# Kernel tuning notes

Hardware: AMD Instinct MI355X
Metric: run time of the kernel (lower is better)

## Reference

```python
import jax, jax.numpy as jnp
import numpy as np

PRIOR = 0.1      # prior_prob
P_NOISE = 0.05   # p
DAMPING = 0.5
BETA = 0.3
EPS = 1e-10


def compute_likelihood(Y_edges, prod_fail_others, beta_edges, p):
    p_sick_if_healthy = 1.0 - prod_fail_others
    p_sick_if_infected = 1.0 - prod_fail_others * (1.0 - beta_edges)
    normal_if_sick = (1.0 - p) * p_sick_if_healthy
    sick_if_sick = (1.0 - p) * p_sick_if_infected
    normal_if_normal = p * p_sick_if_healthy + (1.0 - p_sick_if_healthy)
    sick_if_normal = p * p_sick_if_infected + (1.0 - p_sick_if_infected)
    is_pos = Y_edges == 1
    L0 = jnp.where(is_pos, normal_if_sick, normal_if_normal)
    L1 = jnp.where(is_pos, sick_if_sick, sick_if_normal)
    return L0, L1


def setup_inputs() -> dict:
    key = jax.random.key(0)
    k1, k2, k3 = jax.random.split(key, 3)
    num_tests = 100000
    num_patients = 200000
    num_edges = 12800000
    Y_obs = jax.random.randint(k1, (num_tests,), 0, 2, dtype=jnp.int32)
    idx_i = jax.random.randint(k2, (num_edges,), 0, num_tests, dtype=jnp.int32)
    idx_j = jax.random.randint(k3, (num_edges,), 0, num_patients, dtype=jnp.int32)
    # beta_edges = 1.0 on diagonal entries, beta elsewhere (as in __init__)
    beta_edges = jnp.where(idx_i == idx_j, 1.0, BETA).astype(jnp.float32)
    return {"Y_obs": Y_obs, "idx_i": idx_i, "idx_j": idx_j,
            "beta_edges": beta_edges, "max_iters": 50,
            "num_patients": num_patients}


def reference(Y_obs, idx_i, idx_j, beta_edges, max_iters, num_patients):
    num_tests = Y_obs.shape[0]
    num_edges = idx_i.shape[0]
    Y_edges = Y_obs[idx_i]  # [E]

    def step(carry, it):
        msg_j_to_i, old0, old1, _ = carry
        # test-side aggregation: prob all other patients failed to infect test i
        fail = 1.0 - beta_edges * msg_j_to_i
        log_fail = jnp.log(fail + EPS)
        tot_log_fail = jax.ops.segment_sum(log_fail, idx_i, num_segments=num_tests)
        prod_fail_others = jnp.exp(tot_log_fail[idx_i]) / (fail + EPS)
        new0, new1 = compute_likelihood(Y_edges, prod_fail_others, beta_edges, P_NOISE)
        first = it == 0
        m0 = jnp.where(first, new0, DAMPING * new0 + (1.0 - DAMPING) * old0)
        m1 = jnp.where(first, new1, DAMPING * new1 + (1.0 - DAMPING) * old1)
        old0_n, old1_n = m0, m1  # stored BEFORE normalization, as in torch code
        norm = m0 + m1 + EPS
        log_m0 = jnp.log(m0 / norm + EPS)
        log_m1 = jnp.log(m1 / norm + EPS)
        # patient-side aggregation
        t0 = jax.ops.segment_sum(log_m0, idx_j, num_segments=num_patients)
        t1 = jax.ops.segment_sum(log_m1, idx_j, num_segments=num_patients)
        log_b0 = jnp.log(1.0 - PRIOR) + t0
        log_b1 = jnp.log(PRIOR) + t1
        beliefs = jax.nn.sigmoid(log_b1 - log_b0)  # = 1/(1+exp(lb0-lb1))
        msg_next = jax.nn.sigmoid((log_b1[idx_j] - log_m1) - (log_b0[idx_j] - log_m0))
        return (msg_next, old0_n, old1_n, beliefs), None

    init = (jnp.full((num_edges,), PRIOR, dtype=jnp.float32),
            jnp.zeros((num_edges,), jnp.float32),
            jnp.zeros((num_edges,), jnp.float32),
            jnp.full((num_patients,), PRIOR, dtype=jnp.float32))
    (_, _, _, node_beliefs), _ = jax.lax.scan(step, init, jnp.arange(max_iters))
    return node_beliefs
```

## Files before the change

### kernel.cpp

```cpp
#include <hip/hip_runtime.h>
#include <hip/hip_fp16.h>

#define EPSF   1e-10f
#define PRIORF 0.1f
#define QF     0.95f
#define BETAF  0.3f
#define BS     256
#define WPB    4
#define CAPT   4
#define LOGIT_PRIOR (-2.1972245773362196f)
#define GSH    13
#define NG_MAX 32
#define SPAN_I 256
#define NB2_MAX 1024
#define SPAN_J 128
#define NBJ_MAX 2048
#define CHA    8192
#define CHB    8192
#define CHJ    8192
#define D16    0x2000u
#define JL16   0x1FFFu
#define NXCD   8
#define BSP    1024
#define WPBP   32
#define BLK_SLP 256

__device__ __forceinline__ float wave_sum(float v) {
    #pragma unroll
    for (int m = 32; m >= 1; m >>= 1) v += __shfl_xor(v, m, 64);
    return v;
}
__device__ __forceinline__ float frcp(float x) {
    return __builtin_amdgcn_rcpf(x);
}
__device__ __forceinline__ float2 unpack(__half2 h) {
    return make_float2(__low2float(h), __high2float(h));
}
__device__ __forceinline__ float calcD(float2 o) {
    float inv = frcp(o.x + o.y + EPSF);
    return __logf(o.y * inv + EPSF) - __logf(o.x * inv + EPSF);
}
__device__ __forceinline__ float sigmoidf(float x) {
    return frcp(1.0f + __expf(-x));
}

__device__ __forceinline__ int run_search(int cum, int len, int v0,
                                          int cidx, int NG, int* gout) {
    int lo = 0, hi = NG - 1;
    #pragma unroll
    for (int st = 0; st < 5; ++st) {
        int mid = (lo + hi) >> 1;
        int cmid = __shfl(cum, mid);
        int open = (lo < hi);
        int p = (cmid > cidx);
        int nhi = p ? mid : hi;
        int nlo = p ? lo : (mid + 1);
        hi = open ? nhi : hi;
        lo = open ? nlo : lo;
    }
    int cl = __shfl(cum, lo);
    int ll = __shfl(len, lo);
    int vv = __shfl(v0, lo);
    *gout = lo;
    return vv + cidx - (cl - ll);
}

__global__ __launch_bounds__(BS) void k_test(
    const int*            __restrict__ rowptrG,
    const unsigned short* __restrict__ jidx16,
    const int*            __restrict__ Y,
    const float*          __restrict__ delta,
    __half2*              __restrict__ oldm,
    int T, int NG, int first, int BPC)
{
    int lane = threadIdx.x & 63;
    int x  = blockIdx.x & (NXCD - 1);
    int mm = blockIdx.x >> 3;
    int i = (x * BPC + mm) * WPB + (threadIdx.x >> 6);
    if (i >= T) return;
    int v0 = 0, v1 = 0;
    if (lane < NG) v0 = rowptrG[(size_t)i * NG + lane];
    int l2 = lane - 32;
    if (l2 >= 0 && l2 < NG) v1 = rowptrG[(size_t)(i + 1) * NG + l2];
    int endv = __shfl(v1, 32 + lane);
    int len = (lane < NG) ? (endv - v0) : 0;
    int cum = len;
    #pragma unroll
    for (int off = 1; off < 64; off <<= 1) {
        int t = __shfl_up(cum, off);
        if (lane >= off) cum += t;
    }
    int deg = __shfl(cum, 63);
    int nch = (deg + 63) >> 6;
    int ypos = (Y[i] == 1);
    float lsum = 0.0f;

    if (deg <= 64 * CAPT) {
        int ssv[CAPT]; int ksv[CAPT]; float2 osv[CAPT]; float fsv[CAPT];
        #pragma unroll
        for (int c = 0; c < CAPT; ++c) {
            if (c >= nch) break;
            int idx = c * 64 + lane;
            int cidx = min(idx, deg - 1);
            int g;
            int s = run_search(cum, len, v0, cidx, NG, &g);
            bool act = (idx < deg);
            int k = 0; float2 o = make_float2(0.f, 0.f); float f = 1.0f;
            if (act) {
                k = jidx16[s];
                float b = (k & D16) ? 1.0f : BETAF;
                float msg;
                if (first) msg = PRIORF;
                else {
                    o = unpack(oldm[s]);
                    int j = (g << GSH) | (k & JL16);
                    msg = sigmoidf(delta[j] - calcD(o));
                }
                f = 1.0f - b * msg;
                lsum += __logf(f + EPSF);
            }
            ssv[c] = act ? s : -1; ksv[c] = k; osv[c] = o; fsv[c] = f;
        }
        float Etot = __expf(wave_sum(lsum));
        #pragma unroll
        for (int c = 0; c < CAPT; ++c) {
            if (c >= nch) break;
            int s = ssv[c];
            if (s < 0) continue;
            int k = ksv[c]; float f = fsv[c];
            float b = (k & D16) ? 1.0f : BETAF;
            float prod = Etot * frcp(f + EPSF);
            float psh = 1.0f - prod;
            float psi = 1.0f - prod * (1.0f - b);
            float L0 = ypos ? QF * psh : 1.0f - QF * psh;
            float L1 = ypos ? QF * psi : 1.0f - QF * psi;
            float m0, m1;
            if (first) { m0 = L0; m1 = L1; }
            else { float2 o = osv[c]; m0 = 0.5f * L0 + 0.5f * o.x;
                                      m1 = 0.5f * L1 + 0.5f * o.y; }
            oldm[s] = __floats2half2_rn(m0, m1);
        }
    } else {
        for (int base = 0; base < deg; base += 64) {
            int idx = base + lane;
            int cidx = min(idx, deg - 1);
            int g;
            int s = run_search(cum, len, v0, cidx, NG, &g);
            if (idx < deg) {
                int k = jidx16[s];
                float b = (k & D16) ? 1.0f : BETAF;
                float msg;
                if (first) msg = PRIORF;
                else {
                    int j = (g << GSH) | (k & JL16);
                    msg = sigmoidf(delta[j] - calcD(unpack(oldm[s])));
                }
                lsum += __logf(1.0f - b * msg + EPSF);
            }
        }
        float Etot = __expf(wave_sum(lsum));
        for (int base = 0; base < deg; base += 64) {
            int idx = base + lane;
            int cidx = min(idx, deg - 1);
            int g;
            int s = run_search(cum, len, v0, cidx, NG, &g);
            if (idx < deg) {
                int k = jidx16[s];
                float b = (k & D16) ? 1.0f : BETAF;
                float2 o = make_float2(0.f, 0.f);
                float msg;
                if (first) msg = PRIORF;
                else { o = unpack(oldm[s]);
                       int j = (g << GSH) | (k & JL16);
                       msg = sigmoidf(delta[j] - calcD(o)); }
                float f = 1.0f - b * msg;
                float prod = Etot * frcp(f + EPSF);
                float psh = 1.0f - prod;
                float psi = 1.0f - prod * (1.0f - b);
                float L0 = ypos ? QF * psh : 1.0f - QF * psh;
                float L1 = ypos ? QF * psi : 1.0f - QF * psi;
                float m0, m1;
                if (first) { m0 = L0; m1 = L1; }
                else { m0 = 0.5f * L0 + 0.5f * o.x; m1 = 0.5f * L1 + 0.5f * o.y; }
                oldm[s] = __floats2half2_rn(m0, m1);
            }
        }
    }
}

__global__ __launch_bounds__(BSP) void k_patient(
    const int*     __restrict__ colptr,
    const int*     __restrict__ eposJ,
    const __half2* __restrict__ oldm,
    float*         __restrict__ delta,
    float*         __restrict__ out, int P, int NG)
{
    int b = blockIdx.x;
    int x = b & (NXCD - 1);
    int r = b >> 3;
    int m = r >> 8;
    int w = r & (BLK_SLP - 1);
    int g = x + NXCD * m;
    if (g >= NG) return;
    int lane = threadIdx.x & 63;
    int hl = lane & 31;
    int p = (g << GSH) + w * WPBP + ((threadIdx.x >> 6) << 1) + (lane >> 5);
    if (p >= P) return;
    int u0 = colptr[p], u1 = colptr[p + 1];
    float S = 0.0f;
    for (int u = u0 + hl; u < u1; u += 32)
        S += calcD(unpack(oldm[eposJ[u]]));
    #pragma unroll
    for (int mm = 16; mm >= 1; mm >>= 1) S += __shfl_xor(S, mm, 64);
    if (hl == 0) {
        float d = LOGIT_PRIOR + S;
        delta[p] = d;
        out[p] = sigmoidf(d);
    }
}

__global__ void k_zf2(int* frontG, int* front2, int* frontJ,
                      int NG, int nb2tot, int nbj) {
    int t = blockIdx.x * blockDim.x + threadIdx.x;
    if (t <= NG) frontG[t] = 0;
    if (t <= nb2tot) front2[t] = 0;
    if (t <= nbj) frontJ[t] = 0;
}

__global__ __launch_bounds__(BS) void k_binG(
    const int* __restrict__ idx_i, const int* __restrict__ idx_j,
    int* __restrict__ frontG, unsigned* __restrict__ stageA,
    int E, int NG, int capA)
{
    __shared__ int h[NG_MAX], rsv[NG_MAX], cu[NG_MAX];
    int tid = threadIdx.x;
    if (tid < NG) h[tid] = 0;
    __syncthreads();
    int start = blockIdx.x * CHA, end = min(start + CHA, E);
    for (int e = start + tid; e < end; e += BS)
        atomicAdd(&h[idx_j[e] >> GSH], 1);
    __syncthreads();
    if (tid < NG) { int c = h[tid];
        rsv[tid] = c ? atomicAdd(&frontG[tid], c) : 0; cu[tid] = 0; }
    __syncthreads();
    for (int e = start + tid; e < end; e += BS) {
        int i = idx_i[e], j = idx_j[e];
        int g = j >> GSH;
        int pos = rsv[g] + atomicAdd(&cu[g], 1);
        if (pos < capA)
            stageA[(size_t)g * capA + pos] =
                ((unsigned)i << 14) | ((unsigned)(i == j) << 13)
                | (unsigned)(j & ((1 << GSH) - 1));
    }
}

__global__ __launch_bounds__(BS) void k_binI2(
    const unsigned* __restrict__ stageA, const int* __restrict__ frontG,
    int* __restrict__ front2, unsigned* __restrict__ stage2,
    int NG, int NB2, int capA, int cap2, int chunks)
{
    int g = blockIdx.x / chunks, c = blockIdx.x % chunks;
    int n = min(frontG[g], capA);
    int start = c * 2 * CHB, end = min(start + 2 * CHB, n);
    if (start >= end) return;
    __shared__ int h[NB2_MAX], rsv[NB2_MAX], cu[NB2_MAX];
    int tid = threadIdx.x;
    for (int b = tid; b < NB2; b += BS) h[b] = 0;
    __syncthreads();
    const unsigned* rb = stageA + (size_t)g * capA;
    for (int r = start + tid; r < end; r += BS)
        atomicAdd(&h[(rb[r] >> 14) >> 8], 1);
    __syncthreads();
    for (int b = tid; b < NB2; b += BS) {
        int cc = h[b];
        rsv[b] = cc ? atomicAdd(&front2[g * NB2 + b], cc) : 0;
        cu[b] = 0;
    }
    __syncthreads();
    for (int r = start + tid; r < end; r += BS) {
        unsigned v = rb[r];
        int i = (int)(v >> 14);
        int ib = i >> 8;
        int pos = rsv[ib] + atomicAdd(&cu[ib], 1);
        if (pos < cap2)
            stage2[(size_t)(g * NB2 + ib) * cap2 + pos] =
                ((unsigned)(i & 255) << 14) | (v & 0x3FFFu);
    }
}

__global__ void k_scan_front(int* a, int n, int cap) {
    __shared__ int tmp[BS];
    __shared__ int carry;
    int tid = threadIdx.x;
    if (tid == 0) carry = 0;
    __syncthreads();
    for (int base = 0; base < n; base += BS) {
        int i = base + tid;
        int v = (i < n) ? min(a[i], cap) : 0;
        tmp[tid] = v; __syncthreads();
        for (int off = 1; off < BS; off <<= 1) {
            int x = (tid >= off) ? tmp[tid - off] : 0;
            __syncthreads();
            tmp[tid] += x;
            __syncthreads();
        }
        int c = carry;
        if (i < n) a[i] = c + tmp[tid] - v;
        __syncthreads();
        if (tid == BS - 1) carry = c + tmp[tid];
        __syncthreads();
    }
    if (tid == 0) a[n] = carry;
}

__global__ __launch_bounds__(BS) void k_csr2(
    const unsigned* __restrict__ stage2, const int* __restrict__ front2s,
    int* __restrict__ rowptrG, unsigned short* __restrict__ jidx16,
    int T, int NG, int NB2, int cap2)
{
    __shared__ int deg[SPAN_I], loff[SPAN_I], cu[SPAN_I];
    int b = blockIdx.x, tid = threadIdx.x;
    int g = b / NB2, ib = b % NB2;
    int base = front2s[b];
    int n = min(front2s[b + 1] - base, cap2);
    deg[tid] = 0;
    __syncthreads();
    const unsigned* rb = stage2 + (size_t)b * cap2;
    for (int r = tid; r < n; r += BS)
        atomicAdd(&deg[rb[r] >> 14], 1);
    __syncthreads();
    loff[tid] = deg[tid];
    __syncthreads();
    for (int off = 1; off < SPAN_I; off <<= 1) {
        int v = (tid >= off) ? loff[tid - off] : 0;
        __syncthreads();
        loff[tid] += v;
        __syncthreads();
    }
    {
        int excl = loff[tid] - deg[tid];
        int i = ib * SPAN_I + tid;
        if (i < T) rowptrG[(size_t)i * NG + g] = base + excl;
        cu[tid] = base + excl;
    }
    __syncthreads();
    for (int r = tid; r < n; r += BS) {
        unsigned v = rb[r];
        int pos = atomicAdd(&cu[v >> 14], 1);
        jidx16[pos] = (unsigned short)(v & 0x3FFFu);
    }
}

__global__ void k_fin(const int* front2s, int* rowptrG, int T, int NG, int NB2) {
    int g = threadIdx.x;
    if (g < NG) rowptrG[(size_t)T * NG + g] = front2s[(g + 1) * NB2];
}

__global__ __launch_bounds__(BS) void k_binJ(
    const unsigned short* __restrict__ jidx16,
    const int* __restrict__ front2s,
    int* __restrict__ front, unsigned int* __restrict__ stage,
    int E, int nbj, int cap, int NG, int NB2)
{
    __shared__ int h[NBJ_MAX], rsv[NBJ_MAX], cu[NBJ_MAX];
    __shared__ int ends[NG_MAX];
    int tid = threadIdx.x;
    if (tid < NG) ends[tid] = front2s[(tid + 1) * NB2];
    for (int b = tid; b < nbj; b += BS) h[b] = 0;
    __syncthreads();
    int start = blockIdx.x * CHJ, end = min(start + CHJ, E);
    for (int e = start + tid; e < end; e += BS) {
        int lo = 0, hi = NG - 1;
        while (lo < hi) { int mid = (lo + hi) >> 1;
                          if (e < ends[mid]) hi = mid; else lo = mid + 1; }
        int j = (lo << GSH) | (jidx16[e] & JL16);
        atomicAdd(&h[j >> 7], 1);
    }
    __syncthreads();
    for (int b = tid; b < nbj; b += BS) {
        int c = h[b];
        rsv[b] = c ? atomicAdd(&front[b], c) : 0;
        cu[b] = 0;
    }
    __syncthreads();
    for (int e = start + tid; e < end; e += BS) {
        int lo = 0, hi = NG - 1;
        while (lo < hi) { int mid = (lo + hi) >> 1;
                          if (e < ends[mid]) hi = mid; else lo = mid + 1; }
        int j = (lo << GSH) | (jidx16[e] & JL16);
        int bb = j >> 7;
        int pos = rsv[bb] + atomicAdd(&cu[bb], 1);
        if (pos < cap)
            stage[(size_t)bb * cap + pos] = ((unsigned)(j & 127) << 24) | (unsigned)e;
    }
}

__global__ __launch_bounds__(BS) void k_csrJ(
    const unsigned int* __restrict__ stage, const int* __restrict__ fbase,
    int* __restrict__ colptr, int* __restrict__ eposJ, int P, int E, int cap)
{
    __shared__ int deg[SPAN_J], loff[SPAN_J], cu[SPAN_J];
    int b = blockIdx.x, tid = threadIdx.x;
    int gbase = fbase[b];
    int n = min(fbase[b + 1] - gbase, cap);
    if (tid < SPAN_J) deg[tid] = 0;
    __syncthreads();
    const unsigned int* rb = stage + (size_t)b * cap;
    for (int r = tid; r < n; r += BS)
        atomicAdd(&deg[rb[r] >> 24], 1);
    __syncthreads();
    if (tid < SPAN_J) loff[tid] = deg[tid];
    __syncthreads();
    for (int off = 1; off < SPAN_J; off <<= 1) {
        int v = 0;
        if (tid < SPAN_J && tid >= off) v = loff[tid - off];
        __syncthreads();
        if (tid < SPAN_J) loff[tid] += v;
        __syncthreads();
    }
    if (tid < SPAN_J) {
        int excl = loff[tid] - deg[tid];
        int p = b * SPAN_J + tid;
        if (p < P) colptr[p] = gbase + excl;
        cu[tid] = gbase + excl;
    }
    __syncthreads();
    for (int r = tid; r < n; r += BS) {
        unsigned int v = rb[r];
        int pos = atomicAdd(&cu[v >> 24], 1);
        eposJ[pos] = (int)(v & 0xFFFFFFu);
    }
    if (b == 0 && tid == 0) colptr[P] = E;
}

extern "C" void kernel_launch(void* const* d_in, const int* in_sizes, int n_in,
                              void* d_out, int out_size, void* d_ws, size_t ws_size,
                              hipStream_t stream) {
    const int* Y     = (const int*)d_in[0];
    const int* idx_i = (const int*)d_in[1];
    const int* idx_j = (const int*)d_in[2];
    const int T = in_sizes[0];
    const int E = in_sizes[1];
    const int P = out_size;
    const int ITERS = 50;

    int* eposJ = (int*)d_in[3];

    const int NG     = (P + (1 << GSH) - 1) >> GSH;
    const int NB2    = (T + SPAN_I - 1) / SPAN_I;
    const int nb2tot = NG * NB2;
    const int nbj    = (P + SPAN_J - 1) / SPAN_J;
    long long meanA = (long long)E * (1 << GSH) / P;
    const int capA  = (int)(meanA + (meanA >> 6) + 4096);
    long long mean2 = meanA * SPAN_I / T;
    const int cap2  = (int)(mean2 + (mean2 >> 4) + 256);
    const int capJ  = E / nbj + E / (nbj * 8) + 1024;

    char* ws = (char*)d_ws;
    auto alloc = [&](size_t bytes) -> char* {
        char* p = ws; ws += (bytes + 255) & ~(size_t)255; return p;
    };
    int* rowptrG = (int*)alloc((size_t)(T + 1) * NG * 4);
    int* colptr  = (int*)alloc((size_t)(P + 1) * 4);
    int* frontG  = (int*)alloc((size_t)(NG + 1) * 4);
    int* front2  = (int*)alloc((size_t)(nb2tot + 1) * 4);
    int* frontJ  = (int*)alloc((size_t)(nbj + 1) * 4);
    size_t szA = (size_t)capA * NG * 4, szjx = (size_t)E * 2;
    char* regionA = alloc(szA > szjx ? szA : szjx);
    unsigned*       stageA = (unsigned*)regionA;
    unsigned short* jidx16 = (unsigned short*)regionA;
    size_t oldm_b = ((size_t)E * 4 + 255) & ~(size_t)255;
    size_t sz2 = (size_t)cap2 * nb2tot * 4;
    size_t szJ = (size_t)capJ * nbj * 4;
    size_t szO = oldm_b + (size_t)P * 4;
    size_t szB = sz2 > szJ ? sz2 : szJ; if (szO > szB) szB = szO;
    char* regionB = alloc(szB);
    unsigned* stage2 = (unsigned*)regionB;
    unsigned* stageJ = (unsigned*)regionB;
    __half2*  oldm   = (__half2*)regionB;
    float*    delta  = (float*)(regionB + oldm_b);
    float*    out    = (float*)d_out;

    const int zb = (nb2tot + BS) / BS + 1;
    const int chunks = (capA + 2 * CHB - 1) / (2 * CHB);
    k_zf2<<<zb, BS, 0, stream>>>(frontG, front2, frontJ, NG, nb2tot, nbj);
    k_binG<<<(E + CHA - 1) / CHA, BS, 0, stream>>>(idx_i, idx_j, frontG, stageA,
                                                   E, NG, capA);
    k_binI2<<<NG * chunks, BS, 0, stream>>>(stageA, frontG, front2, stage2,
                                            NG, NB2, capA, cap2, chunks);
    k_scan_front<<<1, BS, 0, stream>>>(front2, nb2tot, cap2);
    k_csr2<<<nb2tot, BS, 0, stream>>>(stage2, front2, rowptrG, jidx16,
                                      T, NG, NB2, cap2);
    k_fin<<<1, 64, 0, stream>>>(front2, rowptrG, T, NG, NB2);
    k_binJ<<<(E + CHJ - 1) / CHJ, BS, 0, stream>>>(jidx16, front2, frontJ, stageJ,
                                                   E, nbj, capJ, NG, NB2);
    k_scan_front<<<1, BS, 0, stream>>>(frontJ, nbj, capJ);
    k_csrJ<<<nbj, BS, 0, stream>>>(stageJ, frontJ, colptr, eposJ, P, E, capJ);

    const int BPC   = (T + WPB * NXCD - 1) / (WPB * NXCD);
    const int tgrid = NXCD * BPC;
    const int maxm  = (NG + NXCD - 1) / NXCD;
    const int pgrid = NXCD * maxm * BLK_SLP;
    for (int it = 0; it < ITERS; ++it) {
        k_test<<<tgrid, BS, 0, stream>>>(rowptrG, jidx16, Y, delta, oldm,
                                         T, NG, it == 0, BPC);
        k_patient<<<pgrid, BSP, 0, stream>>>(colptr, eposJ, oldm, delta, out,
                                             P, NG);
    }
}
```

Before: 8.482 ms.

## Precompute per-edge patient messages in patient kernel and pack diagonal flags into bits

The patient kernel now makes a second pass over each patient's edges and writes a per-edge float prem = belief logit minus own message. The test kernel then reads that value directly instead of gathering delta[j] at random and decoding jidx16. Diagonal flags are compacted into a bitmask so jidx16 no longer has to be read each iteration, and its buffer is reused to hold prem. The cost is an extra scattered write of E floats plus a re-read of oldm in the patient kernel, in exchange for removing the random delta gather. CHB is also doubled.

```diff
diff --git a/kernel.cpp b/kernel.cpp
--- a/kernel.cpp
+++ b/kernel.cpp
@@ -16,7 +16,7 @@
 #define SPAN_J 128
 #define NBJ_MAX 2048
 #define CHA    8192
-#define CHB    8192
+#define CHB    16384
 #define CHJ    8192
 #define D16    0x2000u
 #define JL16   0x1FFFu
@@ -66,11 +66,11 @@
 }
 
 __global__ __launch_bounds__(BS) void k_test(
-    const int*            __restrict__ rowptrG,
-    const unsigned short* __restrict__ jidx16,
-    const int*            __restrict__ Y,
-    const float*          __restrict__ delta,
-    __half2*              __restrict__ oldm,
+    const int*      __restrict__ rowptrG,
+    const unsigned* __restrict__ diagbits,
+    const float*    __restrict__ prem,
+    const int*      __restrict__ Y,
+    __half2*        __restrict__ oldm,
     int T, int NG, int first, int BPC)
 {
     int lane = threadIdx.x & 63;
@@ -96,7 +96,7 @@
     float lsum = 0.0f;
 
     if (deg <= 64 * CAPT) {
-        int ssv[CAPT]; int ksv[CAPT]; float2 osv[CAPT]; float fsv[CAPT];
+        int ssv[CAPT]; unsigned kv[CAPT]; float fsv[CAPT];
         #pragma unroll
         for (int c = 0; c < CAPT; ++c) {
             if (c >= nch) break;
@@ -105,21 +105,17 @@
             int g;
             int s = run_search(cum, len, v0, cidx, NG, &g);
             bool act = (idx < deg);
-            int k = 0; float2 o = make_float2(0.f, 0.f); float f = 1.0f;
+            unsigned diag = 0; float f = 1.0f;
             if (act) {
-                k = jidx16[s];
-                float b = (k & D16) ? 1.0f : BETAF;
+                diag = (diagbits[s >> 5] >> (s & 31)) & 1u;
+                float b = diag ? 1.0f : BETAF;
                 float msg;
                 if (first) msg = PRIORF;
-                else {
-                    o = unpack(oldm[s]);
-                    int j = (g << GSH) | (k & JL16);
-                    msg = sigmoidf(delta[j] - calcD(o));
-                }
+                else       msg = sigmoidf(prem[s]);
                 f = 1.0f - b * msg;
                 lsum += __logf(f + EPSF);
             }
-            ssv[c] = act ? s : -1; ksv[c] = k; osv[c] = o; fsv[c] = f;
+            ssv[c] = act ? s : -1; kv[c] = diag; fsv[c] = f;
         }
         float Etot = __expf(wave_sum(lsum));
         #pragma unroll
@@ -127,8 +123,8 @@
             if (c >= nch) break;
             int s = ssv[c];
             if (s < 0) continue;
-            int k = ksv[c]; float f = fsv[c];
-            float b = (k & D16) ? 1.0f : BETAF;
+            float f = fsv[c];
+            float b = kv[c] ? 1.0f : BETAF;
             float prod = Etot * frcp(f + EPSF);
             float psh = 1.0f - prod;
             float psi = 1.0f - prod * (1.0f - b);
@@ -136,8 +132,9 @@
             float L1 = ypos ? QF * psi : 1.0f - QF * psi;
             float m0, m1;
             if (first) { m0 = L0; m1 = L1; }
-            else { float2 o = osv[c]; m0 = 0.5f * L0 + 0.5f * o.x;
-                                      m1 = 0.5f * L1 + 0.5f * o.y; }
+            else { float2 o = unpack(oldm[s]);
+                   m0 = 0.5f * L0 + 0.5f * o.x;
+                   m1 = 0.5f * L1 + 0.5f * o.y; }
             oldm[s] = __floats2half2_rn(m0, m1);
         }
     } else {
@@ -147,14 +144,11 @@
             int g;
             int s = run_search(cum, len, v0, cidx, NG, &g);
             if (idx < deg) {
-                int k = jidx16[s];
-                float b = (k & D16) ? 1.0f : BETAF;
+                unsigned diag = (diagbits[s >> 5] >> (s & 31)) & 1u;
+                float b = diag ? 1.0f : BETAF;
                 float msg;
                 if (first) msg = PRIORF;
-                else {
-                    int j = (g << GSH) | (k & JL16);
-                    msg = sigmoidf(delta[j] - calcD(unpack(oldm[s])));
-                }
+                else       msg = sigmoidf(prem[s]);
                 lsum += __logf(1.0f - b * msg + EPSF);
             }
         }
@@ -165,14 +159,11 @@
             int g;
             int s = run_search(cum, len, v0, cidx, NG, &g);
             if (idx < deg) {
-                int k = jidx16[s];
-                float b = (k & D16) ? 1.0f : BETAF;
-                float2 o = make_float2(0.f, 0.f);
+                unsigned diag = (diagbits[s >> 5] >> (s & 31)) & 1u;
+                float b = diag ? 1.0f : BETAF;
                 float msg;
                 if (first) msg = PRIORF;
-                else { o = unpack(oldm[s]);
-                       int j = (g << GSH) | (k & JL16);
-                       msg = sigmoidf(delta[j] - calcD(o)); }
+                else       msg = sigmoidf(prem[s]);
                 float f = 1.0f - b * msg;
                 float prod = Etot * frcp(f + EPSF);
                 float psh = 1.0f - prod;
@@ -181,7 +172,8 @@
                 float L1 = ypos ? QF * psi : 1.0f - QF * psi;
                 float m0, m1;
                 if (first) { m0 = L0; m1 = L1; }
-                else { m0 = 0.5f * L0 + 0.5f * o.x; m1 = 0.5f * L1 + 0.5f * o.y; }
+                else { float2 o = unpack(oldm[s]);
+                       m0 = 0.5f * L0 + 0.5f * o.x; m1 = 0.5f * L1 + 0.5f * o.y; }
                 oldm[s] = __floats2half2_rn(m0, m1);
             }
         }
@@ -192,7 +184,7 @@
     const int*     __restrict__ colptr,
     const int*     __restrict__ eposJ,
     const __half2* __restrict__ oldm,
-    float*         __restrict__ delta,
+    float*         __restrict__ prem,
     float*         __restrict__ out, int P, int NG)
 {
     int b = blockIdx.x;
@@ -212,10 +204,11 @@
         S += calcD(unpack(oldm[eposJ[u]]));
     #pragma unroll
     for (int mm = 16; mm >= 1; mm >>= 1) S += __shfl_xor(S, mm, 64);
-    if (hl == 0) {
-        float d = LOGIT_PRIOR + S;
-        delta[p] = d;
-        out[p] = sigmoidf(d);
+    float d = LOGIT_PRIOR + S;
+    if (hl == 0) out[p] = sigmoidf(d);
+    for (int u = u0 + hl; u < u1; u += 32) {
+        int s = eposJ[u];
+        prem[s] = d - calcD(unpack(oldm[s]));
     }
 }
 
@@ -356,6 +349,16 @@
     if (g < NG) rowptrG[(size_t)T * NG + g] = front2s[(g + 1) * NB2];
 }
 
+__global__ __launch_bounds__(BS) void k_bits(
+    const unsigned short* __restrict__ jidx16,
+    unsigned long long*   __restrict__ diagbits64, int E)
+{
+    int e = blockIdx.x * BS + threadIdx.x;
+    unsigned short v = (e < E) ? jidx16[e] : (unsigned short)0;
+    unsigned long long m = __ballot((v >> 13) & 1);
+    if ((threadIdx.x & 63) == 0 && e < E) diagbits64[e >> 6] = m;
+}
+
 __global__ __launch_bounds__(BS) void k_binJ(
     const unsigned short* __restrict__ jidx16,
     const int* __restrict__ front2s,
@@ -465,20 +468,23 @@
     int* frontG  = (int*)alloc((size_t)(NG + 1) * 4);
     int* front2  = (int*)alloc((size_t)(nb2tot + 1) * 4);
     int* frontJ  = (int*)alloc((size_t)(nbj + 1) * 4);
-    size_t szA = (size_t)capA * NG * 4, szjx = (size_t)E * 2;
-    char* regionA = alloc(szA > szjx ? szA : szjx);
+    char* dbp = alloc((((size_t)E + 63) / 64) * 8);
+    unsigned long long* diagbits64 = (unsigned long long*)dbp;
+    unsigned*           diagbits32 = (unsigned*)dbp;
+    size_t szA = (size_t)capA * NG * 4, szjx = (size_t)E * 2, szpr = (size_t)E * 4;
+    size_t szRA = szA > szjx ? szA : szjx; if (szpr > szRA) szRA = szpr;
+    char* regionA = alloc(szRA);
     unsigned*       stageA = (unsigned*)regionA;
     unsigned short* jidx16 = (unsigned short*)regionA;
-    size_t oldm_b = ((size_t)E * 4 + 255) & ~(size_t)255;
+    float*          prem   = (float*)regionA;
+    size_t oldm_b = (size_t)E * 4;
     size_t sz2 = (size_t)cap2 * nb2tot * 4;
     size_t szJ = (size_t)capJ * nbj * 4;
-    size_t szO = oldm_b + (size_t)P * 4;
-    size_t szB = sz2 > szJ ? sz2 : szJ; if (szO > szB) szB = szO;
+    size_t szB = sz2 > szJ ? sz2 : szJ; if (oldm_b > szB) szB = oldm_b;
     char* regionB = alloc(szB);
     unsigned* stage2 = (unsigned*)regionB;
     unsigned* stageJ = (unsigned*)regionB;
     __half2*  oldm   = (__half2*)regionB;
-    float*    delta  = (float*)(regionB + oldm_b);
     float*    out    = (float*)d_out;
 
     const int zb = (nb2tot + BS) / BS + 1;
@@ -496,15 +502,16 @@
                                                    E, nbj, capJ, NG, NB2);
     k_scan_front<<<1, BS, 0, stream>>>(frontJ, nbj, capJ);
     k_csrJ<<<nbj, BS, 0, stream>>>(stageJ, frontJ, colptr, eposJ, P, E, capJ);
+    k_bits<<<(E + BS - 1) / BS, BS, 0, stream>>>(jidx16, diagbits64, E);
 
     const int BPC   = (T + WPB * NXCD - 1) / (WPB * NXCD);
     const int tgrid = NXCD * BPC;
     const int maxm  = (NG + NXCD - 1) / NXCD;
     const int pgrid = NXCD * maxm * BLK_SLP;
     for (int it = 0; it < ITERS; ++it) {
-        k_test<<<tgrid, BS, 0, stream>>>(rowptrG, jidx16, Y, delta, oldm,
+        k_test<<<tgrid, BS, 0, stream>>>(rowptrG, diagbits32, prem, Y, oldm,
                                          T, NG, it == 0, BPC);
-        k_patient<<<pgrid, BSP, 0, stream>>>(colptr, eposJ, oldm, delta, out,
+        k_patient<<<pgrid, BSP, 0, stream>>>(colptr, eposJ, oldm, prem, out,
                                              P, NG);
     }
 }
```

Result: slower. 15.14 ms (+78.5%).

## Process tests in 256-row blocks with shared-memory delta tiles and LDS atomics

Applied to the files above, without the earlier changes.

Replaces the wave-per-test kernel with a block that handles 256 tests at once. For each patient group it stages the delta slice (8192 floats) into shared memory and walks that group's edges in order, accumulating per-test log sums with shared-memory atomics through a new per-edge 8-bit local test index. The goal is to drop the per-edge binary search and turn random global delta gathers into LDS reads. In exchange it adds an extra byte array written during CSR build, repeated delta tile loads per block and group (done twice), LDS atomic contention, and many block-wide syncs. CHB is also doubled.

```diff
diff --git a/kernel.cpp b/kernel.cpp
--- a/kernel.cpp
+++ b/kernel.cpp
@@ -6,8 +6,8 @@
 #define QF     0.95f
 #define BETAF  0.3f
 #define BS     256
-#define WPB    4
-#define CAPT   4
+#define BST    1024
+#define TPB2   256
 #define LOGIT_PRIOR (-2.1972245773362196f)
 #define GSH    13
 #define NG_MAX 32
@@ -16,7 +16,7 @@
 #define SPAN_J 128
 #define NBJ_MAX 2048
 #define CHA    8192
-#define CHB    8192
+#define CHB    16384
 #define CHJ    8192
 #define D16    0x2000u
 #define JL16   0x1FFFu
@@ -25,11 +25,6 @@
 #define WPBP   32
 #define BLK_SLP 256
 
-__device__ __forceinline__ float wave_sum(float v) {
-    #pragma unroll
-    for (int m = 32; m >= 1; m >>= 1) v += __shfl_xor(v, m, 64);
-    return v;
-}
 __device__ __forceinline__ float frcp(float x) {
     return __builtin_amdgcn_rcpf(x);
 }
@@ -44,147 +39,87 @@
     return frcp(1.0f + __expf(-x));
 }
 
-__device__ __forceinline__ int run_search(int cum, int len, int v0,
-                                          int cidx, int NG, int* gout) {
-    int lo = 0, hi = NG - 1;
-    #pragma unroll
-    for (int st = 0; st < 5; ++st) {
-        int mid = (lo + hi) >> 1;
-        int cmid = __shfl(cum, mid);
-        int open = (lo < hi);
-        int p = (cmid > cidx);
-        int nhi = p ? mid : hi;
-        int nlo = p ? lo : (mid + 1);
-        hi = open ? nhi : hi;
-        lo = open ? nlo : lo;
-    }
-    int cl = __shfl(cum, lo);
-    int ll = __shfl(len, lo);
-    int vv = __shfl(v0, lo);
-    *gout = lo;
-    return vv + cidx - (cl - ll);
-}
-
-__global__ __launch_bounds__(BS) void k_test(
+__global__ __launch_bounds__(BST) void k_test2(
     const int*            __restrict__ rowptrG,
     const unsigned short* __restrict__ jidx16,
+    const unsigned char*  __restrict__ ilocal8,
     const int*            __restrict__ Y,
     const float*          __restrict__ delta,
     __half2*              __restrict__ oldm,
-    int T, int NG, int first, int BPC)
-{
-    int lane = threadIdx.x & 63;
-    int x  = blockIdx.x & (NXCD - 1);
-    int mm = blockIdx.x >> 3;
-    int i = (x * BPC + mm) * WPB + (threadIdx.x >> 6);
-    if (i >= T) return;
-    int v0 = 0, v1 = 0;
-    if (lane < NG) v0 = rowptrG[(size_t)i * NG + lane];
-    int l2 = lane - 32;
-    if (l2 >= 0 && l2 < NG) v1 = rowptrG[(size_t)(i + 1) * NG + l2];
-    int endv = __shfl(v1, 32 + lane);
-    int len = (lane < NG) ? (endv - v0) : 0;
-    int cum = len;
-    #pragma unroll
-    for (int off = 1; off < 64; off <<= 1) {
-        int t = __shfl_up(cum, off);
-        if (lane >= off) cum += t;
-    }
-    int deg = __shfl(cum, 63);
-    int nch = (deg + 63) >> 6;
-    int ypos = (Y[i] == 1);
-    float lsum = 0.0f;
-
-    if (deg <= 64 * CAPT) {
-        int ssv[CAPT]; int ksv[CAPT]; float2 osv[CAPT]; float fsv[CAPT];
-        #pragma unroll
-        for (int c = 0; c < CAPT; ++c) {
-            if (c >= nch) break;
-            int idx = c * 64 + lane;
-            int cidx = min(idx, deg - 1);
-            int g;
-            int s = run_search(cum, len, v0, cidx, NG, &g);
-            bool act = (idx < deg);
-            int k = 0; float2 o = make_float2(0.f, 0.f); float f = 1.0f;
-            if (act) {
-                k = jidx16[s];
-                float b = (k & D16) ? 1.0f : BETAF;
-                float msg;
-                if (first) msg = PRIORF;
-                else {
-                    o = unpack(oldm[s]);
-                    int j = (g << GSH) | (k & JL16);
-                    msg = sigmoidf(delta[j] - calcD(o));
-                }
-                f = 1.0f - b * msg;
-                lsum += __logf(f + EPSF);
-            }
-            ssv[c] = act ? s : -1; ksv[c] = k; osv[c] = o; fsv[c] = f;
+    int T, int NG, int P, int first, int BPB)
+{
+    __shared__ float dl[1 << GSH];
+    __shared__ float ls[TPB2];
+    __shared__ float et[TPB2];
+    __shared__ int   yb[TPB2];
+    __shared__ int   sgs[NG_MAX], sge[NG_MAX];
+    int tid = threadIdx.x;
+    int x = blockIdx.x & (NXCD - 1), mm = blockIdx.x >> 3;
+    int ib = x * BPB + mm;
+    int i0 = ib * TPB2;
+    if (i0 >= T) return;
+    int i1 = min(i0 + TPB2, T);
+    if (tid < NG) {
+        sgs[tid] = rowptrG[(size_t)i0 * NG + tid];
+        sge[tid] = rowptrG[(size_t)i1 * NG + tid];
+    }
+    if (tid < TPB2) {
+        ls[tid] = 0.0f;
+        yb[tid] = (i0 + tid < T) ? (Y[i0 + tid] == 1) : 0;
+    }
+    __syncthreads();
+
+    for (int g = 0; g < NG; ++g) {
+        if (!first) {
+            int jb = g << GSH;
+            for (int t = tid; t < (1 << GSH); t += BST)
+                dl[t] = (jb + t < P) ? delta[jb + t] : 0.0f;
+            __syncthreads();
         }
-        float Etot = __expf(wave_sum(lsum));
-        #pragma unroll
-        for (int c = 0; c < CAPT; ++c) {
-            if (c >= nch) break;
-            int s = ssv[c];
-            if (s < 0) continue;
-            int k = ksv[c]; float f = fsv[c];
+        int s0 = sgs[g], s1 = sge[g];
+        for (int s = s0 + tid; s < s1; s += BST) {
+            int k  = jidx16[s];
+            int il = ilocal8[s];
             float b = (k & D16) ? 1.0f : BETAF;
-            float prod = Etot * frcp(f + EPSF);
+            float msg = first ? PRIORF
+                : sigmoidf(dl[k & JL16] - calcD(unpack(oldm[s])));
+            atomicAdd(&ls[il], __logf(1.0f - b * msg + EPSF));
+        }
+        __syncthreads();
+    }
+    if (tid < TPB2) et[tid] = __expf(ls[tid]);
+    __syncthreads();
+
+    for (int g = 0; g < NG; ++g) {
+        if (!first) {
+            int jb = g << GSH;
+            for (int t = tid; t < (1 << GSH); t += BST)
+                dl[t] = (jb + t < P) ? delta[jb + t] : 0.0f;
+            __syncthreads();
+        }
+        int s0 = sgs[g], s1 = sge[g];
+        for (int s = s0 + tid; s < s1; s += BST) {
+            int k  = jidx16[s];
+            int il = ilocal8[s];
+            float b = (k & D16) ? 1.0f : BETAF;
+            float2 o = make_float2(0.f, 0.f);
+            float msg;
+            if (first) msg = PRIORF;
+            else { o = unpack(oldm[s]);
+                   msg = sigmoidf(dl[k & JL16] - calcD(o)); }
+            float f = 1.0f - b * msg;
+            float prod = et[il] * frcp(f + EPSF);
             float psh = 1.0f - prod;
             float psi = 1.0f - prod * (1.0f - b);
-            float L0 = ypos ? QF * psh : 1.0f - QF * psh;
-            float L1 = ypos ? QF * psi : 1.0f - QF * psi;
+            int yp = yb[il];
+            float L0 = yp ? QF * psh : 1.0f - QF * psh;
+            float L1 = yp ? QF * psi : 1.0f - QF * psi;
             float m0, m1;
             if (first) { m0 = L0; m1 = L1; }
-            else { float2 o = osv[c]; m0 = 0.5f * L0 + 0.5f * o.x;
-                                      m1 = 0.5f * L1 + 0.5f * o.y; }
+            else { m0 = 0.5f * L0 + 0.5f * o.x; m1 = 0.5f * L1 + 0.5f * o.y; }
             oldm[s] = __floats2half2_rn(m0, m1);
         }
-    } else {
-        for (int base = 0; base < deg; base += 64) {
-            int idx = base + lane;
-            int cidx = min(idx, deg - 1);
-            int g;
-            int s = run_search(cum, len, v0, cidx, NG, &g);
-            if (idx < deg) {
-                int k = jidx16[s];
-                float b = (k & D16) ? 1.0f : BETAF;
-                float msg;
-                if (first) msg = PRIORF;
-                else {
-                    int j = (g << GSH) | (k & JL16);
-                    msg = sigmoidf(delta[j] - calcD(unpack(oldm[s])));
-                }
-                lsum += __logf(1.0f - b * msg + EPSF);
-            }
-        }
-        float Etot = __expf(wave_sum(lsum));
-        for (int base = 0; base < deg; base += 64) {
-            int idx = base + lane;
-            int cidx = min(idx, deg - 1);
-            int g;
-            int s = run_search(cum, len, v0, cidx, NG, &g);
-            if (idx < deg) {
-                int k = jidx16[s];
-                float b = (k & D16) ? 1.0f : BETAF;
-                float2 o = make_float2(0.f, 0.f);
-                float msg;
-                if (first) msg = PRIORF;
-                else { o = unpack(oldm[s]);
-                       int j = (g << GSH) | (k & JL16);
-                       msg = sigmoidf(delta[j] - calcD(o)); }
-                float f = 1.0f - b * msg;
-                float prod = Etot * frcp(f + EPSF);
-                float psh = 1.0f - prod;
-                float psi = 1.0f - prod * (1.0f - b);
-                float L0 = ypos ? QF * psh : 1.0f - QF * psh;
-                float L1 = ypos ? QF * psi : 1.0f - QF * psi;
-                float m0, m1;
-                if (first) { m0 = L0; m1 = L1; }
-                else { m0 = 0.5f * L0 + 0.5f * o.x; m1 = 0.5f * L1 + 0.5f * o.y; }
-                oldm[s] = __floats2half2_rn(m0, m1);
-            }
-        }
+        __syncthreads();
     }
 }
 
@@ -316,6 +251,7 @@
 __global__ __launch_bounds__(BS) void k_csr2(
     const unsigned* __restrict__ stage2, const int* __restrict__ front2s,
     int* __restrict__ rowptrG, unsigned short* __restrict__ jidx16,
+    unsigned char* __restrict__ ilocal8,
     int T, int NG, int NB2, int cap2)
 {
     __shared__ int deg[SPAN_I], loff[SPAN_I], cu[SPAN_I];
@@ -347,7 +283,8 @@
     for (int r = tid; r < n; r += BS) {
         unsigned v = rb[r];
         int pos = atomicAdd(&cu[v >> 14], 1);
-        jidx16[pos] = (unsigned short)(v & 0x3FFFu);
+        jidx16[pos]  = (unsigned short)(v & 0x3FFFu);
+        ilocal8[pos] = (unsigned char)(v >> 14);
     }
 }
 
@@ -465,6 +402,7 @@
     int* frontG  = (int*)alloc((size_t)(NG + 1) * 4);
     int* front2  = (int*)alloc((size_t)(nb2tot + 1) * 4);
     int* frontJ  = (int*)alloc((size_t)(nbj + 1) * 4);
+    unsigned char* ilocal8 = (unsigned char*)alloc((size_t)E);
     size_t szA = (size_t)capA * NG * 4, szjx = (size_t)E * 2;
     char* regionA = alloc(szA > szjx ? szA : szjx);
     unsigned*       stageA = (unsigned*)regionA;
@@ -489,7 +427,7 @@
     k_binI2<<<NG * chunks, BS, 0, stream>>>(stageA, frontG, front2, stage2,
                                             NG, NB2, capA, cap2, chunks);
     k_scan_front<<<1, BS, 0, stream>>>(front2, nb2tot, cap2);
-    k_csr2<<<nb2tot, BS, 0, stream>>>(stage2, front2, rowptrG, jidx16,
+    k_csr2<<<nb2tot, BS, 0, stream>>>(stage2, front2, rowptrG, jidx16, ilocal8,
                                       T, NG, NB2, cap2);
     k_fin<<<1, 64, 0, stream>>>(front2, rowptrG, T, NG, NB2);
     k_binJ<<<(E + CHJ - 1) / CHJ, BS, 0, stream>>>(jidx16, front2, frontJ, stageJ,
@@ -497,13 +435,13 @@
     k_scan_front<<<1, BS, 0, stream>>>(frontJ, nbj, capJ);
     k_csrJ<<<nbj, BS, 0, stream>>>(stageJ, frontJ, colptr, eposJ, P, E, capJ);
 
-    const int BPC   = (T + WPB * NXCD - 1) / (WPB * NXCD);
-    const int tgrid = NXCD * BPC;
-    const int maxm  = (NG + NXCD - 1) / NXCD;
-    const int pgrid = NXCD * maxm * BLK_SLP;
+    const int BPB    = (NB2 + NXCD - 1) / NXCD;
+    const int tgrid2 = NXCD * BPB;
+    const int maxm   = (NG + NXCD - 1) / NXCD;
+    const int pgrid  = NXCD * maxm * BLK_SLP;
     for (int it = 0; it < ITERS; ++it) {
-        k_test<<<tgrid, BS, 0, stream>>>(rowptrG, jidx16, Y, delta, oldm,
-                                         T, NG, it == 0, BPC);
+        k_test2<<<tgrid2, BST, 0, stream>>>(rowptrG, jidx16, ilocal8, Y, delta,
+                                            oldm, T, NG, P, it == 0, BPB);
         k_patient<<<pgrid, BSP, 0, stream>>>(colptr, eposJ, oldm, delta, out,
                                              P, NG);
     }
```

After: 15.29 ms. 80.3% more time.
